# Kernel optimization log

Hardware: AMD Instinct MI355X
Metric: run time of the kernel (lower is better)

Reference implementation:

```python
import jax, jax.numpy as jnp
import numpy as np

HILBERT_BITS = 8
NDIM = 3


def hilbert_distance(grid, bits=HILBERT_BITS):
    """Vectorized Skilling transform: grid [..., 3] int32 in [0, 2**bits-1] -> Hilbert index [...] int32.
    Exact port of hilbertcurve.HilbertCurve.distance_from_point (n=3, p=bits)."""
    x = [grid[..., i] for i in range(NDIM)]
    m = 1 << (bits - 1)
    # Inverse undo excess work
    q = m
    while q > 1:
        pm = q - 1
        for i in range(NDIM):
            cond = (x[i] & q) != 0
            if i == 0:
                x[0] = jnp.where(cond, x[0] ^ pm, x[0])
            else:
                t = (x[0] ^ x[i]) & pm
                x0n = jnp.where(cond, x[0] ^ pm, x[0] ^ t)
                xin = jnp.where(cond, x[i], x[i] ^ t)
                x[0], x[i] = x0n, xin
        q >>= 1
    # Gray encode
    x[1] = x[1] ^ x[0]
    x[2] = x[2] ^ x[1]
    t = jnp.zeros_like(x[2])
    q = m
    while q > 1:
        t = jnp.where((x[2] & q) != 0, t ^ (q - 1), t)
        q >>= 1
    x = [xi ^ t for xi in x]
    # Interleave bits, MSB first, dim order 0,1,2 -> h has bits*3 bits (24 fits int32)
    h = jnp.zeros_like(x[0])
    for bpos in range(bits - 1, -1, -1):
        for i in range(NDIM):
            h = (h << 1) | ((x[i] >> bpos) & 1)
    return h


def hilbert_orders(x, bits=HILBERT_BITS):
    # x: [B, N, 3] float. Per-batch min/max normalization, then quantize to grid.
    mins = x.min(axis=1, keepdims=True)
    maxs = x.max(axis=1, keepdims=True)
    span = jnp.maximum(maxs - mins, 1e-6)
    norm = (x - mins) / span
    mx = (1 << bits) - 1
    grid_h = jnp.clip(norm * mx, 0, mx).astype(jnp.int32)
    grid_t = jnp.clip(norm[..., ::-1] * mx, 0, mx).astype(jnp.int32)  # [z,y,x] variant
    order_h = jnp.argsort(hilbert_distance(grid_h, bits), axis=-1)
    order_t = jnp.argsort(hilbert_distance(grid_t, bits), axis=-1)
    return order_h, order_t


def setup_inputs() -> dict:
    key = jax.random.key(0)
    k1, k2, k3 = jax.random.split(key, 3)
    B, N, D = 16, 4096, 384
    x = jax.random.normal(k1, (B, N, 3), dtype=jnp.float32)
    W = jax.random.normal(k2, (D, 3), dtype=jnp.float32) * 0.5
    b = jax.random.normal(k3, (D,), dtype=jnp.float32) * 0.1
    gamma = jnp.ones((2, D), dtype=jnp.float32)
    beta = jnp.zeros((2, D), dtype=jnp.float32)
    return {"x": x, "W": W, "b": b, "gamma": gamma, "beta": beta}


def reference(x, W, b, gamma, beta):
    order_h, order_t = hilbert_orders(x)                     # [B, N] each
    pts_h = jnp.take_along_axis(x, order_h[..., None], axis=1)  # [B, N, 3]
    pts_t = jnp.take_along_axis(x, order_t[..., None], axis=1)
    base_h = jnp.einsum('bnc,dc->bnd', pts_h, W) + b         # Linear(3, D)
    base_t = jnp.einsum('bnc,dc->bnd', pts_t, W) + b
    tokens_h = base_h * gamma[0] + beta[0]
    tokens_t = base_t * gamma[1] + beta[1]
    return jnp.concatenate([tokens_h, tokens_t], axis=1)     # [B, 2N, D]
```

## Files before the change

### kernel.cpp

```cpp
#include <hip/hip_runtime.h>
#include <stdint.h>

#define BATCH 16
#define NPTS 4096
#define DIM 384
#define NTOK (2*NPTS)
#define F4PT (DIM/4)

typedef unsigned long long u64;

__device__ __forceinline__ uint32_t spread3(uint32_t x) {
    x = (x | (x << 8)) & 0x00F00Fu;
    x = (x | (x << 4)) & 0x0C30C3u;
    x = (x | (x << 2)) & 0x249249u;
    return x;
}

__device__ __forceinline__ uint32_t hilbert3(uint32_t x0, uint32_t x1, uint32_t x2) {
    #pragma unroll
    for (uint32_t q = 128; q > 1; q >>= 1) {
        uint32_t pm = q - 1;
        if (x0 & q) x0 ^= pm;
        uint32_t t = (x0 ^ x1) & pm;
        if (x1 & q) { x0 ^= pm; } else { x0 ^= t; x1 ^= t; }
        t = (x0 ^ x2) & pm;
        if (x2 & q) { x0 ^= pm; } else { x0 ^= t; x2 ^= t; }
    }
    x1 ^= x0;
    x2 ^= x1;
    uint32_t t = 0;
    #pragma unroll
    for (uint32_t q = 128; q > 1; q >>= 1) { if (x2 & q) t ^= (q - 1); }
    x0 ^= t; x1 ^= t; x2 ^= t;
    return (spread3(x0) << 2) | (spread3(x1) << 1) | spread3(x2);
}

__global__ __launch_bounds__(1024) void order_radix_q(const float* __restrict__ x,
                                                      u64* __restrict__ kws) {
    const int bi = blockIdx.x;
    const int b = bi >> 3;
    const int v = (bi >> 2) & 1;
    const int q = bi & 3;
    const int t = threadIdx.x;
    const int lane = t & 63;
    const int w = t >> 6;

    __shared__ u64 skey[1024];
    __shared__ uint32_t hist[16 * 16];
    __shared__ uint32_t binTot[16];
    __shared__ uint32_t baseArr[16];
    __shared__ float red[16 * 6];

    const float* xb = x + (size_t)b * NPTS * 3;

    float px[4], py[4], pz[4];
    #pragma unroll
    for (int g = 0; g < 4; ++g) {
        int n = t + (g << 10);
        px[g] = xb[3*n+0]; py[g] = xb[3*n+1]; pz[g] = xb[3*n+2];
    }

    float mnx = 1e30f, mny = 1e30f, mnz = 1e30f;
    float mxx = -1e30f, mxy = -1e30f, mxz = -1e30f;
    #pragma unroll
    for (int g = 0; g < 4; ++g) {
        mnx = fminf(mnx, px[g]); mxx = fmaxf(mxx, px[g]);
        mny = fminf(mny, py[g]); mxy = fmaxf(mxy, py[g]);
        mnz = fminf(mnz, pz[g]); mxz = fmaxf(mxz, pz[g]);
    }
    #pragma unroll
    for (int off = 32; off > 0; off >>= 1) {
        mnx = fminf(mnx, __shfl_xor(mnx, off));
        mny = fminf(mny, __shfl_xor(mny, off));
        mnz = fminf(mnz, __shfl_xor(mnz, off));
        mxx = fmaxf(mxx, __shfl_xor(mxx, off));
        mxy = fmaxf(mxy, __shfl_xor(mxy, off));
        mxz = fmaxf(mxz, __shfl_xor(mxz, off));
    }
    if (lane == 0) {
        red[w*6+0] = mnx; red[w*6+1] = mny; red[w*6+2] = mnz;
        red[w*6+3] = mxx; red[w*6+4] = mxy; red[w*6+5] = mxz;
    }
    if (t < 256) hist[t] = 0u;
    if (t < 16) binTot[t] = 0u;
    __syncthreads();
    if (t == 0) {
        for (int ww = 1; ww < 16; ++ww) {
            mnx = fminf(mnx, red[ww*6+0]); mny = fminf(mny, red[ww*6+1]);
            mnz = fminf(mnz, red[ww*6+2]); mxx = fmaxf(mxx, red[ww*6+3]);
            mxy = fmaxf(mxy, red[ww*6+4]); mxz = fmaxf(mxz, red[ww*6+5]);
        }
        red[0] = mnx; red[1] = mny; red[2] = mnz;
        red[3] = fmaxf(mxx - mnx, 1e-6f);
        red[4] = fmaxf(mxy - mny, 1e-6f);
        red[5] = fmaxf(mxz - mnz, 1e-6f);
    }
    __syncthreads();
    mnx = red[0]; mny = red[1]; mnz = red[2];
    const float spx = red[3], spy = red[4], spz = red[5];

    u64 key;
    {
        int n = (q << 10) + t;
        float gx = fminf(fmaxf(((px[q] - mnx) / spx) * 255.0f, 0.0f), 255.0f);
        float gy = fminf(fmaxf(((py[q] - mny) / spy) * 255.0f, 0.0f), 255.0f);
        float gz = fminf(fmaxf(((pz[q] - mnz) / spz) * 255.0f, 0.0f), 255.0f);
        uint32_t ix = (uint32_t)(int)gx;
        uint32_t iy = (uint32_t)(int)gy;
        uint32_t iz = (uint32_t)(int)gz;
        uint32_t a0 = v ? iz : ix;
        uint32_t a2 = v ? ix : iz;
        uint32_t code = hilbert3(a0, iy, a2);
        key = ((u64)code << 12) | (u64)n;
    }

    const u64 below_mask = (1ull << lane) - 1ull;
    u64* segk = kws + (((b << 1) | v) << 12);

    #pragma unroll
    for (int p = 0; p < 6; ++p) {
        const int sh = 12 + 4 * p;

        unsigned d = (unsigned)(key >> sh) & 15u;
        u64 m = ~0ull;
        #pragma unroll
        for (int bit = 0; bit < 4; ++bit) {
            u64 bal = __ballot((int)((d >> bit) & 1u));
            m &= ((d >> bit) & 1u) ? bal : ~bal;
        }
        unsigned rk = (unsigned)__popcll(m & below_mask);
        if (rk == 0u) {
            unsigned cnt = (unsigned)__popcll(m);
            hist[d * 16 + w] = cnt;
            atomicAdd(&binTot[d], cnt);
        }
        __syncthreads();

        {
            unsigned val = (lane < 16) ? hist[w * 16 + lane] : 0u;
            unsigned orig = val;
            #pragma unroll
            for (int off = 1; off < 16; off <<= 1) {
                unsigned nv = __shfl_up(val, off);
                if (lane >= off) val += nv;
            }
            if (lane < 16) hist[w * 16 + lane] = val - orig;
        }
        if (w == 0) {
            unsigned tv = (lane < 16) ? binTot[lane] : 0u;
            unsigned orig = tv;
            #pragma unroll
            for (int off = 1; off < 16; off <<= 1) {
                unsigned nv = __shfl_up(tv, off);
                if (lane >= off) tv += nv;
            }
            if (lane < 16) baseArr[lane] = tv - orig;
        }
        __syncthreads();

        unsigned pos = baseArr[d] + hist[d * 16 + w] + rk;

        if (p < 5) {
            skey[pos] = key;
            __syncthreads();
            key = skey[t];
            if (t < 256) hist[t] = 0u;
            if (t < 16) binTot[t] = 0u;
            __syncthreads();
        } else {
            segk[(q << 10) + pos] = key;
        }
    }
}

__global__ __launch_bounds__(1024) void order_merge_q(const u64* __restrict__ kws,
                                                      int* __restrict__ order) {
    const int bi = blockIdx.x;
    const int b = bi >> 3;
    const int v = (bi >> 2) & 1;
    const int q = bi & 3;
    const int t = threadIdx.x;

    __shared__ u64 sk[3][1024];

    const u64* segk = kws + (((b << 1) | v) << 12);
    u64 k = segk[(q << 10) + t];

    #pragma unroll
    for (int j = 0; j < 3; ++j) {
        int oq = j + (j >= q ? 1 : 0);
        sk[j][t] = segk[(oq << 10) + t];
    }
    __syncthreads();

    int rank = t;
    #pragma unroll
    for (int j = 0; j < 3; ++j) {
        int c = 0;
        #pragma unroll
        for (int step = 1024; step >= 1; step >>= 1) {
            if (c + step <= 1024 && sk[j][c + step - 1] < k) c += step;
        }
        rank += c;
    }

    order[(((b << 1) | v) << 12) + rank] = (int)(k & 0xFFFull);
}

__global__ __launch_bounds__(256) void token_kernel(const float* __restrict__ x,
                                                    const float* __restrict__ W,
                                                    const float* __restrict__ bias,
                                                    const float* __restrict__ gamma,
                                                    const float* __restrict__ beta,
                                                    const int* __restrict__ order,
                                                    float* __restrict__ out) {
    __shared__ __align__(16) float sW0[2][DIM];
    __shared__ __align__(16) float sW1[2][DIM];
    __shared__ __align__(16) float sW2[2][DIM];
    __shared__ __align__(16) float sC[2][DIM];
    for (int i = threadIdx.x; i < 2 * DIM; i += 256) {
        int v = i / DIM;
        int d = i - v * DIM;
        float g = gamma[i];
        sW0[v][d] = g * W[d*3+0];
        sW1[v][d] = g * W[d*3+1];
        sW2[v][d] = g * W[d*3+2];
        sC[v][d]  = g * bias[d] + beta[i];
    }
    __syncthreads();

    const int total = BATCH * NTOK * F4PT;
    const int stride = gridDim.x * blockDim.x;
    for (int g4 = blockIdx.x * blockDim.x + threadIdx.x; g4 < total; g4 += stride) {
        int token = g4 / F4PT;
        int grp = g4 - token * F4PT;
        int b = token >> 13;
        int nn = token & (NTOK - 1);
        int v = nn >> 12;
        int n = nn & (NPTS - 1);
        int idx = order[(((b << 1) | v) << 12) + n];
        const float* p = x + (size_t)(b * NPTS + idx) * 3;
        float px = p[0], py = p[1], pz = p[2];
        int d0 = grp << 2;
        float4 w0 = *(const float4*)&sW0[v][d0];
        float4 w1 = *(const float4*)&sW1[v][d0];
        float4 w2 = *(const float4*)&sW2[v][d0];
        float4 c  = *(const float4*)&sC[v][d0];
        float4 o;
        o.x = px*w0.x + py*w1.x + pz*w2.x + c.x;
        o.y = px*w0.y + py*w1.y + pz*w2.y + c.y;
        o.z = px*w0.z + py*w1.z + pz*w2.z + c.z;
        o.w = px*w0.w + py*w1.w + pz*w2.w + c.w;
        reinterpret_cast<float4*>(out)[g4] = o;
    }
}

extern "C" void kernel_launch(void* const* d_in, const int* in_sizes, int n_in,
                              void* d_out, int out_size, void* d_ws, size_t ws_size,
                              hipStream_t stream) {
    const float* x     = (const float*)d_in[0];
    const float* W     = (const float*)d_in[1];
    const float* bias  = (const float*)d_in[2];
    const float* gamma = (const float*)d_in[3];
    const float* beta  = (const float*)d_in[4];

    u64* kws   = (u64*)d_ws;
    int* order = (int*)(kws + 32 * 4096);

    hipLaunchKernelGGL(order_radix_q, dim3(BATCH * 8), dim3(1024), 0, stream, x, kws);
    hipLaunchKernelGGL(order_merge_q, dim3(BATCH * 8), dim3(1024), 0, stream, kws, order);
    hipLaunchKernelGGL(token_kernel,  dim3(2048),      dim3(256),  0, stream,
                       x, W, bias, gamma, beta, order, (float*)d_out);
}
```

Before: 54.89 us.

## Split Hilbert radix sort into eight 512-key segments per batch-view

Each batch/view is now sorted as eight 512-key segments in 256 blocks of 512 threads, instead of four 1024-key segments in 128 blocks. The merge kernel ranks each key by binary search across seven sibling segments rather than three. The min/max pass now uses float4 loads. Per-pass histograms get their own slices and are scanned serially by 16 threads, which removes the atomics and the zeroing sync. The aim is more blocks for better GPU occupancy and shorter radix passes, at the cost of more binary searches in the merge.

```diff
diff --git a/kernel.cpp b/kernel.cpp
--- a/kernel.cpp
+++ b/kernel.cpp
@@ -35,38 +35,40 @@
     return (spread3(x0) << 2) | (spread3(x1) << 1) | spread3(x2);
 }
 
-__global__ __launch_bounds__(1024) void order_radix_q(const float* __restrict__ x,
-                                                      u64* __restrict__ kws) {
+__global__ __launch_bounds__(512) void order_radix_o(const float* __restrict__ x,
+                                                     u64* __restrict__ kws) {
     const int bi = blockIdx.x;
-    const int b = bi >> 3;
-    const int v = (bi >> 2) & 1;
-    const int q = bi & 3;
+    const int b = bi >> 4;
+    const int v = (bi >> 3) & 1;
+    const int oct = bi & 7;
     const int t = threadIdx.x;
     const int lane = t & 63;
     const int w = t >> 6;
 
-    __shared__ u64 skey[1024];
-    __shared__ uint32_t hist[16 * 16];
-    __shared__ uint32_t binTot[16];
+    __shared__ u64 skey[512];
+    __shared__ uint32_t hist[6 * 128];
     __shared__ uint32_t baseArr[16];
-    __shared__ float red[16 * 6];
+    __shared__ float red[8 * 6];
 
     const float* xb = x + (size_t)b * NPTS * 3;
-
-    float px[4], py[4], pz[4];
-    #pragma unroll
-    for (int g = 0; g < 4; ++g) {
-        int n = t + (g << 10);
-        px[g] = xb[3*n+0]; py[g] = xb[3*n+1]; pz[g] = xb[3*n+2];
-    }
+    const float4* xb4 = (const float4*)xb;
 
     float mnx = 1e30f, mny = 1e30f, mnz = 1e30f;
     float mxx = -1e30f, mxy = -1e30f, mxz = -1e30f;
     #pragma unroll
-    for (int g = 0; g < 4; ++g) {
-        mnx = fminf(mnx, px[g]); mxx = fmaxf(mxx, px[g]);
-        mny = fminf(mny, py[g]); mxy = fmaxf(mxy, py[g]);
-        mnz = fminf(mnz, pz[g]); mxz = fmaxf(mxz, pz[g]);
+    for (int h = 0; h < 2; ++h) {
+        float4 q0 = xb4[h * 1536 + 3 * t + 0];
+        float4 q1 = xb4[h * 1536 + 3 * t + 1];
+        float4 q2 = xb4[h * 1536 + 3 * t + 2];
+        float px[4] = {q0.x, q0.w, q1.z, q2.y};
+        float py[4] = {q0.y, q1.x, q1.w, q2.z};
+        float pz[4] = {q0.z, q1.y, q2.x, q2.w};
+        #pragma unroll
+        for (int r = 0; r < 4; ++r) {
+            mnx = fminf(mnx, px[r]); mxx = fmaxf(mxx, px[r]);
+            mny = fminf(mny, py[r]); mxy = fmaxf(mxy, py[r]);
+            mnz = fminf(mnz, pz[r]); mxz = fmaxf(mxz, pz[r]);
+        }
     }
     #pragma unroll
     for (int off = 32; off > 0; off >>= 1) {
@@ -81,11 +83,11 @@
         red[w*6+0] = mnx; red[w*6+1] = mny; red[w*6+2] = mnz;
         red[w*6+3] = mxx; red[w*6+4] = mxy; red[w*6+5] = mxz;
     }
-    if (t < 256) hist[t] = 0u;
-    if (t < 16) binTot[t] = 0u;
+    hist[t] = 0u;
+    if (t < 256) hist[512 + t] = 0u;
     __syncthreads();
     if (t == 0) {
-        for (int ww = 1; ww < 16; ++ww) {
+        for (int ww = 1; ww < 8; ++ww) {
             mnx = fminf(mnx, red[ww*6+0]); mny = fminf(mny, red[ww*6+1]);
             mnz = fminf(mnz, red[ww*6+2]); mxx = fmaxf(mxx, red[ww*6+3]);
             mxy = fmaxf(mxy, red[ww*6+4]); mxz = fmaxf(mxz, red[ww*6+5]);
@@ -101,17 +103,18 @@
 
     u64 key;
     {
-        int n = (q << 10) + t;
-        float gx = fminf(fmaxf(((px[q] - mnx) / spx) * 255.0f, 0.0f), 255.0f);
-        float gy = fminf(fmaxf(((py[q] - mny) / spy) * 255.0f, 0.0f), 255.0f);
-        float gz = fminf(fmaxf(((pz[q] - mnz) / spz) * 255.0f, 0.0f), 255.0f);
+        const int n0 = (oct << 9) + t;
+        float cx = xb[3*n0+0], cy = xb[3*n0+1], cz = xb[3*n0+2];
+        float gx = fminf(fmaxf(((cx - mnx) / spx) * 255.0f, 0.0f), 255.0f);
+        float gy = fminf(fmaxf(((cy - mny) / spy) * 255.0f, 0.0f), 255.0f);
+        float gz = fminf(fmaxf(((cz - mnz) / spz) * 255.0f, 0.0f), 255.0f);
         uint32_t ix = (uint32_t)(int)gx;
         uint32_t iy = (uint32_t)(int)gy;
         uint32_t iz = (uint32_t)(int)gz;
         uint32_t a0 = v ? iz : ix;
         uint32_t a2 = v ? ix : iz;
         uint32_t code = hilbert3(a0, iy, a2);
-        key = ((u64)code << 12) | (u64)n;
+        key = ((u64)code << 12) | (u64)n0;
     }
 
     const u64 below_mask = (1ull << lane) - 1ull;
@@ -120,6 +123,7 @@
     #pragma unroll
     for (int p = 0; p < 6; ++p) {
         const int sh = 12 + 4 * p;
+        uint32_t* histp = hist + p * 128;
 
         unsigned d = (unsigned)(key >> sh) & 15u;
         u64 m = ~0ull;
@@ -129,77 +133,68 @@
             m &= ((d >> bit) & 1u) ? bal : ~bal;
         }
         unsigned rk = (unsigned)__popcll(m & below_mask);
-        if (rk == 0u) {
-            unsigned cnt = (unsigned)__popcll(m);
-            hist[d * 16 + w] = cnt;
-            atomicAdd(&binTot[d], cnt);
-        }
+        if (rk == 0u)
+            histp[d * 8 + w] = (unsigned)__popcll(m);
         __syncthreads();
 
-        {
-            unsigned val = (lane < 16) ? hist[w * 16 + lane] : 0u;
-            unsigned orig = val;
+        if (t < 16) {
+            unsigned running = 0;
             #pragma unroll
-            for (int off = 1; off < 16; off <<= 1) {
-                unsigned nv = __shfl_up(val, off);
-                if (lane >= off) val += nv;
+            for (int s = 0; s < 8; ++s) {
+                unsigned hv = histp[t * 8 + s];
+                histp[t * 8 + s] = running;
+                running += hv;
             }
-            if (lane < 16) hist[w * 16 + lane] = val - orig;
-        }
-        if (w == 0) {
-            unsigned tv = (lane < 16) ? binTot[lane] : 0u;
-            unsigned orig = tv;
+            unsigned tv = running;
             #pragma unroll
             for (int off = 1; off < 16; off <<= 1) {
                 unsigned nv = __shfl_up(tv, off);
                 if (lane >= off) tv += nv;
             }
-            if (lane < 16) baseArr[lane] = tv - orig;
+            baseArr[t] = tv - running;
         }
         __syncthreads();
 
-        unsigned pos = baseArr[d] + hist[d * 16 + w] + rk;
+        unsigned pos = baseArr[d] + histp[d * 8 + w] + rk;
 
         if (p < 5) {
             skey[pos] = key;
             __syncthreads();
             key = skey[t];
-            if (t < 256) hist[t] = 0u;
-            if (t < 16) binTot[t] = 0u;
-            __syncthreads();
         } else {
-            segk[(q << 10) + pos] = key;
-        }
-    }
-}
-
-__global__ __launch_bounds__(1024) void order_merge_q(const u64* __restrict__ kws,
-                                                      int* __restrict__ order) {
+            segk[(oct << 9) + pos] = key;
+        }
+    }
+}
+
+__global__ __launch_bounds__(512) void order_merge_o(const u64* __restrict__ kws,
+                                                     int* __restrict__ order) {
     const int bi = blockIdx.x;
-    const int b = bi >> 3;
-    const int v = (bi >> 2) & 1;
-    const int q = bi & 3;
+    const int b = bi >> 4;
+    const int v = (bi >> 3) & 1;
+    const int oct = bi & 7;
     const int t = threadIdx.x;
 
-    __shared__ u64 sk[3][1024];
+    __shared__ u64 sk[7 * 512];
 
     const u64* segk = kws + (((b << 1) | v) << 12);
-    u64 k = segk[(q << 10) + t];
-
-    #pragma unroll
-    for (int j = 0; j < 3; ++j) {
-        int oq = j + (j >= q ? 1 : 0);
-        sk[j][t] = segk[(oq << 10) + t];
+    u64 k = segk[(oct << 9) + t];
+
+    #pragma unroll
+    for (int j = 0; j < 7; ++j) {
+        int oq = j + (j >= oct ? 1 : 0);
+        sk[j * 512 + t] = segk[(oq << 9) + t];
     }
     __syncthreads();
 
     int rank = t;
     #pragma unroll
-    for (int j = 0; j < 3; ++j) {
+    for (int j = 0; j < 7; ++j) {
+        const u64* s = &sk[j * 512];
         int c = 0;
         #pragma unroll
-        for (int step = 1024; step >= 1; step >>= 1) {
-            if (c + step <= 1024 && sk[j][c + step - 1] < k) c += step;
+        for (int step = 512; step >= 1; step >>= 1) {
+            if (c + step <= 512 && s[c + step - 1] < k) c += step;
         }
         rank += c;
     }
@@ -267,8 +262,8 @@
     u64* kws   = (u64*)d_ws;
     int* order = (int*)(kws + 32 * 4096);
 
-    hipLaunchKernelGGL(order_radix_q, dim3(BATCH * 8), dim3(1024), 0, stream, x, kws);
-    hipLaunchKernelGGL(order_merge_q, dim3(BATCH * 8), dim3(1024), 0, stream, kws, order);
-    hipLaunchKernelGGL(token_kernel,  dim3(2048),      dim3(256),  0, stream,
+    hipLaunchKernelGGL(order_radix_o, dim3(BATCH * 16), dim3(512), 0, stream, x, kws);
+    hipLaunchKernelGGL(order_merge_o, dim3(BATCH * 16), dim3(512), 0, stream, kws, order);
+    hipLaunchKernelGGL(token_kernel,  dim3(2048),       dim3(256), 0, stream,
                        x, W, bias, gamma, beta, order, (float*)d_out);
 }
```

Measured after the change: 53.90 us. Within noise of the previous version (-1.8%).
